# Kernel optimization log

Hardware: AMD Instinct MI355X
Metric: run time of the kernel (lower is better)

## Reference

```python
import jax, jax.numpy as jnp
import numpy as np


def setup_inputs() -> dict:
    key = jax.random.key(0)
    ks = jax.random.split(key, 13)
    B, T, D, H = 64, 2048, 64, 128
    s_in = 1.0 / np.sqrt(H)  # torch RNN/Linear init scale (uniform bound); use scaled normal
    return {
        "x": jax.random.normal(ks[0], (B, T, D), dtype=jnp.float32),
        "W_ih_f": jax.random.normal(ks[1], (H, D), dtype=jnp.float32) * s_in,
        "W_hh_f": jax.random.normal(ks[2], (H, H), dtype=jnp.float32) * s_in,
        "b_ih_f": jax.random.normal(ks[3], (H,), dtype=jnp.float32) * s_in,
        "b_hh_f": jax.random.normal(ks[4], (H,), dtype=jnp.float32) * s_in,
        "W_ih_b": jax.random.normal(ks[5], (H, D), dtype=jnp.float32) * s_in,
        "W_hh_b": jax.random.normal(ks[6], (H, H), dtype=jnp.float32) * s_in,
        "b_ih_b": jax.random.normal(ks[7], (H,), dtype=jnp.float32) * s_in,
        "b_hh_b": jax.random.normal(ks[8], (H,), dtype=jnp.float32) * s_in,
        "fc1_W": jax.random.normal(ks[9], (H, 2 * H), dtype=jnp.float32) * s_in,
        "fc1_b": jax.random.normal(ks[10], (H,), dtype=jnp.float32) * s_in,
        "fc2_W": jax.random.normal(ks[11], (1, H), dtype=jnp.float32) * s_in,
        "fc2_b": jax.random.normal(ks[12], (1,), dtype=jnp.float32) * s_in,
    }


def _rnn_dir(x_proj, W_hh):
    # x_proj: [T, B, H] = x @ W_ih^T + b_ih + b_hh, precomputed (vectorized part)
    # recurrence: h_t = relu(x_proj_t + h_{t-1} @ W_hh^T)
    T, B, H = x_proj.shape
    h0 = jnp.zeros((B, H), dtype=x_proj.dtype)

    def step(h, xp_t):
        h_new = jax.nn.relu(xp_t + h @ W_hh.T)
        return h_new, h_new

    _, hs = jax.lax.scan(step, h0, x_proj)
    return hs  # [T, B, H]


def reference(x, W_ih_f, W_hh_f, b_ih_f, b_hh_f,
              W_ih_b, W_hh_b, b_ih_b, b_hh_b,
              fc1_W, fc1_b, fc2_W, fc2_b):
    # x: [B, T, D]
    xt = jnp.swapaxes(x, 0, 1)  # [T, B, D]
    # forward direction
    xp_f = jnp.einsum('tbd,hd->tbh', xt, W_ih_f) + b_ih_f + b_hh_f
    hs_f = _rnn_dir(xp_f, W_hh_f)  # [T, B, H]
    # backward direction: run over time-reversed input, then reverse outputs
    xp_b = jnp.einsum('tbd,hd->tbh', xt[::-1], W_ih_b) + b_ih_b + b_hh_b
    hs_b = _rnn_dir(xp_b, W_hh_b)[::-1]  # [T, B, H]
    h = jnp.concatenate([hs_f, hs_b], axis=-1)  # [T, B, 2H]
    h = jnp.swapaxes(h, 0, 1)  # [B, T, 2H]
    h = jnp.einsum('bti,oi->bto', h, fc1_W) + fc1_b  # [B, T, H]
    h = jnp.einsum('bti,oi->bto', h, fc2_W) + fc2_b  # [B, T, 1]
    logits = h[..., 0]  # [B, T]
    return jax.nn.log_softmax(logits, axis=1)
```

## Files before the change

kernel.cpp:

```cpp
#include <hip/hip_runtime.h>
#include <hip/hip_bf16.h>

#define T_LEN 2048
#define B_SZ  64
#define D_IN  64
#define H_SZ  128

__global__ __launch_bounds__(256)
void prep_kernel(const float* __restrict__ fc1_W, const float* __restrict__ fc1_b,
                 const float* __restrict__ fc2_W, const float* __restrict__ fc2_b,
                 float* __restrict__ ws)
{
    const int i = threadIdx.x;
    float s = 0.0f;
    #pragma unroll 4
    for (int o = 0; o < 128; ++o) s = fmaf(fc2_W[o], fc1_W[o * 256 + i], s);
    ws[i] = s;

    __shared__ float red[128];
    if (i < 128) red[i] = fc2_W[i] * fc1_b[i];
    __syncthreads();
    if (i == 0) {
        float b = fc2_b[0];
        for (int o = 0; o < 128; ++o) b += red[o];
        ws[256] = b;
    }
}

#define DPP_ADD_F32(v, ctrl)                                                   \
    v += __int_as_float(__builtin_amdgcn_update_dpp(                           \
            0, __float_as_int(v), (ctrl), 0xf, 0xf, true))

__device__ __forceinline__ void chain_barrier() {
    asm volatile("s_waitcnt lgkmcnt(0)" ::: "memory");
    __builtin_amdgcn_s_barrier();
    __builtin_amdgcn_sched_barrier(0);
}


__global__ __launch_bounds__(256, 1)
void brnn_recur(const float* __restrict__ x,
                const float* __restrict__ Wih_f, const float* __restrict__ Whh_f,
                const float* __restrict__ bih_f, const float* __restrict__ bhh_f,
                const float* __restrict__ Wih_b, const float* __restrict__ Whh_b,
                const float* __restrict__ bih_b, const float* __restrict__ bhh_b,
                const float* __restrict__ weff,  float* __restrict__ partbuf)
{
    const int blk  = blockIdx.x;
    const int dir  = blk >> 6;
    const int b    = blk & 63;
    const int tid  = threadIdx.x;
    const int w    = tid >> 6;
    const int l    = tid & 63;
    const int g    = l & 7;
    const int m    = l >> 3;
    const int j0   = w * 32 + m * 4;
    const bool wr  = (g == 7);

    const float* Wih = dir ? Wih_b : Wih_f;
    const float* Whh = dir ? Whh_b : Whh_f;
    const float* bih = dir ? bih_b : bih_f;
    const float* bhh = dir ? bhh_b : bhh_f;

    float whh[64];
    #pragma unroll
    for (int jj = 0; jj < 4; ++jj)
        #pragma unroll
        for (int i = 0; i < 4; ++i)
            ((float4*)whh)[jj * 4 + i] =
                *(const float4*)(Whh + (j0 + jj) * 128 + g * 16 + i * 4);
    float wih[32];
    #pragma unroll
    for (int jj = 0; jj < 4; ++jj)
        #pragma unroll
        for (int i = 0; i < 2; ++i)
            ((float4*)wih)[jj * 2 + i] =
                *(const float4*)(Wih + (j0 + jj) * 64 + g * 8 + i * 4);

    float4 b4 = make_float4(0.f, 0.f, 0.f, 0.f);
    if (g == 0) {
        float4 bi = *(const float4*)(bih + j0);
        float4 bh = *(const float4*)(bhh + j0);
        b4 = make_float4(bi.x + bh.x, bi.y + bh.y, bi.z + bh.z, bi.w + bh.w);
    }
    const float4 w4 = *(const float4*)(weff + dir * 128 + j0);

    __shared__ __align__(16) float hbuf[2][160];
    if (tid < 160) hbuf[0][tid] = 0.0f;
    __syncthreads();

    const float* xbase = x + (size_t)b * T_LEN * D_IN + g * 8;
    float* pout = partbuf + ((size_t)blk * 4 + w) * T_LEN;

    float xq0[8], xq1[8], xq2[8], xq3[8];
    {
        const float4* xp0 = (const float4*)(xbase + (size_t)(dir ? (T_LEN - 1) : 0) * D_IN);
        ((float4*)xq0)[0] = xp0[0];
        ((float4*)xq0)[1] = xp0[1];
        const float4* xp1 = (const float4*)(xbase + (size_t)(dir ? (T_LEN - 2) : 1) * D_IN);
        ((float4*)xq1)[0] = xp1[0];
        ((float4*)xq1)[1] = xp1[1];
    }

    float p_carry = 0.0f;
    int   t_prev  = 0;

    const int hwidx = 40 * w + 4 * m + 4 * (m >> 2);

#define STEP(S, RD, XCUR, XPRE) do {                                           \
        const int s_  = (S);                                                   \
           \
           \
        if (s_ > 0) {                                                          \
            float pr_ = p_carry;                                               \
            DPP_ADD_F32(pr_, 0x111); DPP_ADD_F32(pr_, 0x112);                  \
            DPP_ADD_F32(pr_, 0x114); DPP_ADD_F32(pr_, 0x118);                  \
            DPP_ADD_F32(pr_, 0x142); DPP_ADD_F32(pr_, 0x143);                  \
            if (l == 63) pout[t_prev] = pr_;                                   \
        }                                                                      \
            \
        {                                                                      \
            const int sp_ = (s_ + 2 < T_LEN) ? (s_ + 2) : (T_LEN - 1);         \
            const int tp_ = dir ? (T_LEN - 1 - sp_) : sp_;                     \
            const float4* xp_ = (const float4*)(xbase + (size_t)tp_ * D_IN);   \
            ((float4*)XPRE)[0] = xp_[0];                                       \
            ((float4*)XPRE)[1] = xp_[1];                                       \
        }                                                                      \
            \
        const float4* hp_ = (const float4*)&hbuf[RD][20 * g];                  \
        float4 hv_[4];                                                         \
        _Pragma("unroll") for (int i = 0; i < 4; ++i) hv_[i] = hp_[i];         \
        float a0 = b4.x, a1 = b4.y, a2 = b4.z, a3 = b4.w;                      \
        _Pragma("unroll") for (int i = 0; i < 8; ++i) {                        \
            a0 = fmaf(wih[0 * 8 + i], XCUR[i], a0);                            \
            a1 = fmaf(wih[1 * 8 + i], XCUR[i], a1);                            \
            a2 = fmaf(wih[2 * 8 + i], XCUR[i], a2);                            \
            a3 = fmaf(wih[3 * 8 + i], XCUR[i], a3);                            \
        }                                                                      \
        _Pragma("unroll") for (int i = 0; i < 4; ++i) {                        \
            const float* hq_ = (const float*)&hv_[i];                          \
            _Pragma("unroll") for (int c = 0; c < 4; ++c) {                    \
                a0 = fmaf(whh[0 * 16 + i * 4 + c], hq_[c], a0);                \
                a1 = fmaf(whh[1 * 16 + i * 4 + c], hq_[c], a1);                \
                a2 = fmaf(whh[2 * 16 + i * 4 + c], hq_[c], a2);                \
                a3 = fmaf(whh[3 * 16 + i * 4 + c], hq_[c], a3);                \
            }                                                                  \
        }                                                                      \
             \
        DPP_ADD_F32(a0, 0x111); DPP_ADD_F32(a1, 0x111);                        \
        DPP_ADD_F32(a2, 0x111); DPP_ADD_F32(a3, 0x111);                        \
        DPP_ADD_F32(a0, 0x112); DPP_ADD_F32(a1, 0x112);                        \
        DPP_ADD_F32(a2, 0x112); DPP_ADD_F32(a3, 0x112);                        \
        DPP_ADD_F32(a0, 0x114); DPP_ADD_F32(a1, 0x114);                        \
        DPP_ADD_F32(a2, 0x114); DPP_ADD_F32(a3, 0x114);                        \
        float4 h4_;                                                            \
        h4_.x = fmaxf(a0, 0.0f); h4_.y = fmaxf(a1, 0.0f);                      \
        h4_.z = fmaxf(a2, 0.0f); h4_.w = fmaxf(a3, 0.0f);                      \
        p_carry = 0.0f;                                                        \
        if (wr) {                                                              \
            *(float4*)&hbuf[(RD) ^ 1][hwidx] = h4_;                            \
            p_carry = w4.x * h4_.x + w4.y * h4_.y                              \
                    + w4.z * h4_.z + w4.w * h4_.w;                             \
        }                                                                      \
        t_prev = dir ? (T_LEN - 1 - s_) : s_;                                  \
        chain_barrier();                                                       \
    } while (0)

    #pragma unroll 1
    for (int s = 0; s < T_LEN; s += 4) {
        STEP(s,     0, xq0, xq2);
        STEP(s + 1, 1, xq1, xq3);
        STEP(s + 2, 0, xq2, xq0);
        STEP(s + 3, 1, xq3, xq1);
    }
#undef STEP

    {
        float pr = p_carry;
        DPP_ADD_F32(pr, 0x111); DPP_ADD_F32(pr, 0x112);
        DPP_ADD_F32(pr, 0x114); DPP_ADD_F32(pr, 0x118);
        DPP_ADD_F32(pr, 0x142); DPP_ADD_F32(pr, 0x143);
        if (l == 63) pout[t_prev] = pr;
    }
}

__global__ __launch_bounds__(256)
void brnn_lsm(const float* __restrict__ partbuf, const float* __restrict__ ws,
              float* __restrict__ out)
{
    const int b   = blockIdx.x;
    const int tid = threadIdx.x;
    __shared__ float lg[T_LEN];
    __shared__ float red[8];

    const float beff = ws[256];

    float lmax = -3.0e38f;
    for (int t = tid; t < T_LEN; t += 256) {
        float s = beff;
        #pragma unroll
        for (int dw = 0; dw < 8; ++dw) {
            const int dir = dw >> 2, wv = dw & 3;
            s += partbuf[(((size_t)(dir * 64 + b)) * 4 + wv) * T_LEN + t];
        }
        lg[t] = s;
        lmax = fmaxf(lmax, s);
    }
    #pragma unroll
    for (int mm = 1; mm <= 32; mm <<= 1) lmax = fmaxf(lmax, __shfl_xor(lmax, mm));
    if ((tid & 63) == 0) red[tid >> 6] = lmax;
    __syncthreads();
    const float bmax = fmaxf(fmaxf(red[0], red[1]), fmaxf(red[2], red[3]));

    float lsum = 0.0f;
    for (int t = tid; t < T_LEN; t += 256) lsum += expf(lg[t] - bmax);
    #pragma unroll
    for (int mm = 1; mm <= 32; mm <<= 1) lsum += __shfl_xor(lsum, mm);
    if ((tid & 63) == 0) red[4 + (tid >> 6)] = lsum;
    __syncthreads();
    const float lse = bmax + logf(red[4] + red[5] + red[6] + red[7]);

    for (int t = tid; t < T_LEN; t += 256)
        out[(size_t)b * T_LEN + t] = lg[t] - lse;
}

extern "C" void kernel_launch(void* const* d_in, const int* in_sizes, int n_in,
                              void* d_out, int out_size, void* d_ws, size_t ws_size,
                              hipStream_t stream)
{
    const float* x     = (const float*)d_in[0];
    const float* Wih_f = (const float*)d_in[1];
    const float* Whh_f = (const float*)d_in[2];
    const float* bih_f = (const float*)d_in[3];
    const float* bhh_f = (const float*)d_in[4];
    const float* Wih_b = (const float*)d_in[5];
    const float* Whh_b = (const float*)d_in[6];
    const float* bih_b = (const float*)d_in[7];
    const float* bhh_b = (const float*)d_in[8];
    const float* fc1_W = (const float*)d_in[9];
    const float* fc1_b = (const float*)d_in[10];
    const float* fc2_W = (const float*)d_in[11];
    const float* fc2_b = (const float*)d_in[12];
    float* out = (float*)d_out;

    float* wsf  = (float*)d_ws;
    float* part = wsf + 512;

    hipLaunchKernelGGL(prep_kernel, dim3(1), dim3(256), 0, stream,
                       fc1_W, fc1_b, fc2_W, fc2_b, wsf);
    hipLaunchKernelGGL(brnn_recur, dim3(128), dim3(256), 0, stream,
                       x, Wih_f, Whh_f, bih_f, bhh_f,
                       Wih_b, Whh_b, bih_b, bhh_b, wsf, part);
    hipLaunchKernelGGL(brnn_lsm, dim3(64), dim3(256), 0, stream,
                       part, wsf, out);
}
```

Before: 800.6 us.

## Precompute input projection in a separate GEMM kernel before the recurrence

Adds an xp_gemm kernel that computes x·W_ih^T + biases for both directions into a large workspace buffer. The recurrent kernel then loads one float4 of precomputed projection per step instead of doing 32 FMAs against x. The aim is to shorten the per-step serial chain. It also trims the p_carry DPP reduction from six to three steps, because only g==7 lanes hold nonzero values. The cost is an extra kernel that writes and later reads about 128 MB of workspace. A fallback to the old fused path runs when the workspace is too small.

```diff
diff --git a/kernel.cpp b/kernel.cpp
--- a/kernel.cpp
+++ b/kernel.cpp
@@ -27,6 +27,56 @@
     }
 }
 
+__global__ __launch_bounds__(128)
+void xp_gemm(const float* __restrict__ x,
+             const float* __restrict__ Wih_f, const float* __restrict__ bih_f,
+             const float* __restrict__ bhh_f,
+             const float* __restrict__ Wih_b, const float* __restrict__ bih_b,
+             const float* __restrict__ bhh_b,
+             float* __restrict__ xp)
+{
+    const int blk = blockIdx.x;
+    const int dir = blk >> 10;
+    const int b   = (blk >> 4) & 63;
+    const int c   = blk & 15;
+    const int j   = threadIdx.x;
+
+    const float* Wih = dir ? Wih_b : Wih_f;
+    const float* bih = dir ? bih_b : bih_f;
+    const float* bhh = dir ? bhh_b : bhh_f;
+
+    __shared__ __align__(16) float xs[128][64];
+    const float4* xsrc = (const float4*)(x + ((size_t)b * T_LEN + c * 128) * D_IN);
+    float4* xdst = (float4*)&xs[0][0];
+    #pragma unroll
+    for (int i = 0; i < 16; ++i) xdst[threadIdx.x + i * 128] = xsrc[threadIdx.x + i * 128];
+
+    float wr[64];
+    #pragma unroll
+    for (int i = 0; i < 16; ++i) ((float4*)wr)[i] = ((const float4*)(Wih + j * 64))[i];
+    const float bj = bih[j] + bhh[j];
+    __syncthreads();
+
+    float* xpo = xp + (((size_t)(dir * 64 + b)) * T_LEN + c * 128) * H_SZ + j;
+    for (int tt = 0; tt < 128; ++tt) {
+        const float4* xr = (const float4*)&xs[tt][0];
+        float a0 = bj, a1 = 0.f, a2 = 0.f, a3 = 0.f;
+        #pragma unroll
+        for (int i = 0; i < 16; i += 4) {
+            float4 v0 = xr[i], v1 = xr[i + 1], v2 = xr[i + 2], v3 = xr[i + 3];
+            a0 = fmaf(wr[4*i+ 0], v0.x, a0); a0 = fmaf(wr[4*i+ 1], v0.y, a0);
+            a0 = fmaf(wr[4*i+ 2], v0.z, a0); a0 = fmaf(wr[4*i+ 3], v0.w, a0);
+            a1 = fmaf(wr[4*i+ 4], v1.x, a1); a1 = fmaf(wr[4*i+ 5], v1.y, a1);
+            a1 = fmaf(wr[4*i+ 6], v1.z, a1); a1 = fmaf(wr[4*i+ 7], v1.w, a1);
+            a2 = fmaf(wr[4*i+ 8], v2.x, a2); a2 = fmaf(wr[4*i+ 9], v2.y, a2);
+            a2 = fmaf(wr[4*i+10], v2.z, a2); a2 = fmaf(wr[4*i+11], v2.w, a2);
+            a3 = fmaf(wr[4*i+12], v3.x, a3); a3 = fmaf(wr[4*i+13], v3.y, a3);
+            a3 = fmaf(wr[4*i+14], v3.z, a3); a3 = fmaf(wr[4*i+15], v3.w, a3);
+        }
+        xpo[(size_t)tt * H_SZ] = (a0 + a1) + (a2 + a3);
+    }
+}
+
 #define DPP_ADD_F32(v, ctrl)                                                   \
     v += __int_as_float(__builtin_amdgcn_update_dpp(                           \
             0, __float_as_int(v), (ctrl), 0xf, 0xf, true))
@@ -39,12 +89,9 @@
 
 
 __global__ __launch_bounds__(256, 1)
-void brnn_recur(const float* __restrict__ x,
-                const float* __restrict__ Wih_f, const float* __restrict__ Whh_f,
-                const float* __restrict__ bih_f, const float* __restrict__ bhh_f,
-                const float* __restrict__ Wih_b, const float* __restrict__ Whh_b,
-                const float* __restrict__ bih_b, const float* __restrict__ bhh_b,
-                const float* __restrict__ weff,  float* __restrict__ partbuf)
+void brnn_recur_xp(const float* __restrict__ xp,
+                   const float* __restrict__ Whh_f, const float* __restrict__ Whh_b,
+                   const float* __restrict__ weff,  float* __restrict__ partbuf)
 {
     const int blk  = blockIdx.x;
     const int dir  = blk >> 6;
@@ -57,10 +104,7 @@
     const int j0   = w * 32 + m * 4;
     const bool wr  = (g == 7);
 
-    const float* Wih = dir ? Wih_b : Wih_f;
     const float* Whh = dir ? Whh_b : Whh_f;
-    const float* bih = dir ? bih_b : bih_f;
-    const float* bhh = dir ? bhh_b : bhh_f;
 
     float whh[64];
     #pragma unroll
@@ -69,74 +113,49 @@
         for (int i = 0; i < 4; ++i)
             ((float4*)whh)[jj * 4 + i] =
                 *(const float4*)(Whh + (j0 + jj) * 128 + g * 16 + i * 4);
-    float wih[32];
-    #pragma unroll
-    for (int jj = 0; jj < 4; ++jj)
-        #pragma unroll
-        for (int i = 0; i < 2; ++i)
-            ((float4*)wih)[jj * 2 + i] =
-                *(const float4*)(Wih + (j0 + jj) * 64 + g * 8 + i * 4);
-
-    float4 b4 = make_float4(0.f, 0.f, 0.f, 0.f);
-    if (g == 0) {
-        float4 bi = *(const float4*)(bih + j0);
-        float4 bh = *(const float4*)(bhh + j0);
-        b4 = make_float4(bi.x + bh.x, bi.y + bh.y, bi.z + bh.z, bi.w + bh.w);
-    }
+
     const float4 w4 = *(const float4*)(weff + dir * 128 + j0);
 
     __shared__ __align__(16) float hbuf[2][160];
     if (tid < 160) hbuf[0][tid] = 0.0f;
     __syncthreads();
 
-    const float* xbase = x + (size_t)b * T_LEN * D_IN + g * 8;
+    const float* xpbase = xp + ((size_t)(dir * 64 + b)) * T_LEN * H_SZ + j0;
     float* pout = partbuf + ((size_t)blk * 4 + w) * T_LEN;
 
-    float xq0[8], xq1[8], xq2[8], xq3[8];
-    {
-        const float4* xp0 = (const float4*)(xbase + (size_t)(dir ? (T_LEN - 1) : 0) * D_IN);
-        ((float4*)xq0)[0] = xp0[0];
-        ((float4*)xq0)[1] = xp0[1];
-        const float4* xp1 = (const float4*)(xbase + (size_t)(dir ? (T_LEN - 2) : 1) * D_IN);
-        ((float4*)xq1)[0] = xp1[0];
-        ((float4*)xq1)[1] = xp1[1];
-    }
+    float4 xq0, xq1, xq2, xq3;
+    xq0 = *(const float4*)(xpbase + (size_t)(dir ? (T_LEN - 1) : 0) * H_SZ);
+    xq1 = *(const float4*)(xpbase + (size_t)(dir ? (T_LEN - 2) : 1) * H_SZ);
 
     float p_carry = 0.0f;
     int   t_prev  = 0;
 
     const int hwidx = 40 * w + 4 * m + 4 * (m >> 2);
 
-#define STEP(S, RD, XCUR, XPRE) do {                                           \
+#define STEP(S, RD, XPC, XPN) do {                                             \
         const int s_  = (S);                                                   \
-           \
-           \
+                 \
         if (s_ > 0) {                                                          \
             float pr_ = p_carry;                                               \
-            DPP_ADD_F32(pr_, 0x111); DPP_ADD_F32(pr_, 0x112);                  \
-            DPP_ADD_F32(pr_, 0x114); DPP_ADD_F32(pr_, 0x118);                  \
-            DPP_ADD_F32(pr_, 0x142); DPP_ADD_F32(pr_, 0x143);                  \
+            DPP_ADD_F32(pr_, 0x118);     \
+            DPP_ADD_F32(pr_, 0x142);         \
+            DPP_ADD_F32(pr_, 0x143);             \
             if (l == 63) pout[t_prev] = pr_;                                   \
         }                                                                      \
-            \
+                                                 \
         {                                                                      \
             const int sp_ = (s_ + 2 < T_LEN) ? (s_ + 2) : (T_LEN - 1);         \
             const int tp_ = dir ? (T_LEN - 1 - sp_) : sp_;                     \
-            const float4* xp_ = (const float4*)(xbase + (size_t)tp_ * D_IN);   \
-            ((float4*)XPRE)[0] = xp_[0];                                       \
-            ((float4*)XPRE)[1] = xp_[1];                                       \
-        }                                                                      \
-            \
+            XPN = *(const float4*)(xpbase + (size_t)tp_ * H_SZ);               \
+        }                                                                      \
+                                        \
         const float4* hp_ = (const float4*)&hbuf[RD][20 * g];                  \
         float4 hv_[4];                                                         \
         _Pragma("unroll") for (int i = 0; i < 4; ++i) hv_[i] = hp_[i];         \
-        float a0 = b4.x, a1 = b4.y, a2 = b4.z, a3 = b4.w;                      \
-        _Pragma("unroll") for (int i = 0; i < 8; ++i) {                        \
-            a0 = fmaf(wih[0 * 8 + i], XCUR[i], a0);                            \
-            a1 = fmaf(wih[1 * 8 + i], XCUR[i], a1);                            \
-            a2 = fmaf(wih[2 * 8 + i], XCUR[i], a2);                            \
-            a3 = fmaf(wih[3 * 8 + i], XCUR[i], a3);                            \
-        }                                                                      \
+        float a0 = (g == 0) ? XPC.x : 0.0f;                                    \
+        float a1 = (g == 0) ? XPC.y : 0.0f;                                    \
+        float a2 = (g == 0) ? XPC.z : 0.0f;                                    \
+        float a3 = (g == 0) ? XPC.w : 0.0f;                                    \
         _Pragma("unroll") for (int i = 0; i < 4; ++i) {                        \
             const float* hq_ = (const float*)&hv_[i];                          \
             _Pragma("unroll") for (int c = 0; c < 4; ++c) {                    \
@@ -177,9 +196,146 @@
 
     {
         float pr = p_carry;
-        DPP_ADD_F32(pr, 0x111); DPP_ADD_F32(pr, 0x112);
-        DPP_ADD_F32(pr, 0x114); DPP_ADD_F32(pr, 0x118);
-        DPP_ADD_F32(pr, 0x142); DPP_ADD_F32(pr, 0x143);
+        DPP_ADD_F32(pr, 0x118);
+        DPP_ADD_F32(pr, 0x142);
+        DPP_ADD_F32(pr, 0x143);
+        if (l == 63) pout[t_prev] = pr;
+    }
+}
+
+__global__ __launch_bounds__(256, 1)
+void brnn_recur_fb(const float* __restrict__ x,
+                   const float* __restrict__ Wih_f, const float* __restrict__ Whh_f,
+                   const float* __restrict__ bih_f, const float* __restrict__ bhh_f,
+                   const float* __restrict__ Wih_b, const float* __restrict__ Whh_b,
+                   const float* __restrict__ bih_b, const float* __restrict__ bhh_b,
+                   const float* __restrict__ weff,  float* __restrict__ partbuf)
+{
+    const int blk  = blockIdx.x;
+    const int dir  = blk >> 6;
+    const int b    = blk & 63;
+    const int tid  = threadIdx.x;
+    const int w    = tid >> 6;
+    const int l    = tid & 63;
+    const int g    = l & 7;
+    const int m    = l >> 3;
+    const int j0   = w * 32 + m * 4;
+    const bool wr  = (g == 7);
+
+    const float* Wih = dir ? Wih_b : Wih_f;
+    const float* Whh = dir ? Whh_b : Whh_f;
+    const float* bih = dir ? bih_b : bih_f;
+    const float* bhh = dir ? bhh_b : bhh_f;
+
+    float whh[64];
+    #pragma unroll
+    for (int jj = 0; jj < 4; ++jj)
+        #pragma unroll
+        for (int i = 0; i < 4; ++i)
+            ((float4*)whh)[jj * 4 + i] =
+                *(const float4*)(Whh + (j0 + jj) * 128 + g * 16 + i * 4);
+    float wih[32];
+    #pragma unroll
+    for (int jj = 0; jj < 4; ++jj)
+        #pragma unroll
+        for (int i = 0; i < 2; ++i)
+            ((float4*)wih)[jj * 2 + i] =
+                *(const float4*)(Wih + (j0 + jj) * 64 + g * 8 + i * 4);
+
+    float4 b4 = make_float4(0.f, 0.f, 0.f, 0.f);
+    if (g == 0) {
+        float4 bi = *(const float4*)(bih + j0);
+        float4 bh = *(const float4*)(bhh + j0);
+        b4 = make_float4(bi.x + bh.x, bi.y + bh.y, bi.z + bh.z, bi.w + bh.w);
+    }
+    const float4 w4 = *(const float4*)(weff + dir * 128 + j0);
+
+    __shared__ __align__(16) float hbuf[2][160];
+    if (tid < 160) hbuf[0][tid] = 0.0f;
+    __syncthreads();
+
+    const float* xbase = x + (size_t)b * T_LEN * D_IN + g * 8;
+    float* pout = partbuf + ((size_t)blk * 4 + w) * T_LEN;
+
+    float xq0[8], xq1[8], xq2[8], xq3[8];
+    {
+        const float4* xp0 = (const float4*)(xbase + (size_t)(dir ? (T_LEN - 1) : 0) * D_IN);
+        ((float4*)xq0)[0] = xp0[0];
+        ((float4*)xq0)[1] = xp0[1];
+        const float4* xp1 = (const float4*)(xbase + (size_t)(dir ? (T_LEN - 2) : 1) * D_IN);
+        ((float4*)xq1)[0] = xp1[0];
+        ((float4*)xq1)[1] = xp1[1];
+    }
+
+    float p_carry = 0.0f;
+    int   t_prev  = 0;
+    const int hwidx = 40 * w + 4 * m + 4 * (m >> 2);
+
+#define STEP(S, RD, XCUR, XPRE) do {                                           \
+        const int s_  = (S);                                                   \
+        if (s_ > 0) {                                                          \
+            float pr_ = p_carry;                                               \
+            DPP_ADD_F32(pr_, 0x118); DPP_ADD_F32(pr_, 0x142);                  \
+            DPP_ADD_F32(pr_, 0x143);                                           \
+            if (l == 63) pout[t_prev] = pr_;                                   \
+        }                                                                      \
+        {                                                                      \
+            const int sp_ = (s_ + 2 < T_LEN) ? (s_ + 2) : (T_LEN - 1);         \
+            const int tp_ = dir ? (T_LEN - 1 - sp_) : sp_;                     \
+            const float4* xp_ = (const float4*)(xbase + (size_t)tp_ * D_IN);   \
+            ((float4*)XPRE)[0] = xp_[0];                                       \
+            ((float4*)XPRE)[1] = xp_[1];                                       \
+        }                                                                      \
+        const float4* hp_ = (const float4*)&hbuf[RD][20 * g];                  \
+        float4 hv_[4];                                                         \
+        _Pragma("unroll") for (int i = 0; i < 4; ++i) hv_[i] = hp_[i];         \
+        float a0 = b4.x, a1 = b4.y, a2 = b4.z, a3 = b4.w;                      \
+        _Pragma("unroll") for (int i = 0; i < 8; ++i) {                        \
+            a0 = fmaf(wih[0 * 8 + i], XCUR[i], a0);                            \
+            a1 = fmaf(wih[1 * 8 + i], XCUR[i], a1);                            \
+            a2 = fmaf(wih[2 * 8 + i], XCUR[i], a2);                            \
+            a3 = fmaf(wih[3 * 8 + i], XCUR[i], a3);                            \
+        }                                                                      \
+        _Pragma("unroll") for (int i = 0; i < 4; ++i) {                        \
+            const float* hq_ = (const float*)&hv_[i];                          \
+            _Pragma("unroll") for (int c = 0; c < 4; ++c) {                    \
+                a0 = fmaf(whh[0 * 16 + i * 4 + c], hq_[c], a0);                \
+                a1 = fmaf(whh[1 * 16 + i * 4 + c], hq_[c], a1);                \
+                a2 = fmaf(whh[2 * 16 + i * 4 + c], hq_[c], a2);                \
+                a3 = fmaf(whh[3 * 16 + i * 4 + c], hq_[c], a3);                \
+            }                                                                  \
+        }                                                                      \
+        DPP_ADD_F32(a0, 0x111); DPP_ADD_F32(a1, 0x111);                        \
+        DPP_ADD_F32(a2, 0x111); DPP_ADD_F32(a3, 0x111);                        \
+        DPP_ADD_F32(a0, 0x112); DPP_ADD_F32(a1, 0x112);                        \
+        DPP_ADD_F32(a2, 0x112); DPP_ADD_F32(a3, 0x112);                        \
+        DPP_ADD_F32(a0, 0x114); DPP_ADD_F32(a1, 0x114);                        \
+        DPP_ADD_F32(a2, 0x114); DPP_ADD_F32(a3, 0x114);                        \
+        float4 h4_;                                                            \
+        h4_.x = fmaxf(a0, 0.0f); h4_.y = fmaxf(a1, 0.0f);                      \
+        h4_.z = fmaxf(a2, 0.0f); h4_.w = fmaxf(a3, 0.0f);                      \
+        p_carry = 0.0f;                                                        \
+        if (wr) {                                                              \
+            *(float4*)&hbuf[(RD) ^ 1][hwidx] = h4_;                            \
+            p_carry = w4.x * h4_.x + w4.y * h4_.y                              \
+                    + w4.z * h4_.z + w4.w * h4_.w;                             \
+        }                                                                      \
+        t_prev = dir ? (T_LEN - 1 - s_) : s_;                                  \
+        chain_barrier();                                                       \
+    } while (0)
+
+    #pragma unroll 1
+    for (int s = 0; s < T_LEN; s += 4) {
+        STEP(s,     0, xq0, xq2);
+        STEP(s + 1, 1, xq1, xq3);
+        STEP(s + 2, 0, xq2, xq0);
+        STEP(s + 3, 1, xq3, xq1);
+    }
+#undef STEP
+
+    {
+        float pr = p_carry;
+        DPP_ADD_F32(pr, 0x118); DPP_ADD_F32(pr, 0x142); DPP_ADD_F32(pr, 0x143);
         if (l == 63) pout[t_prev] = pr;
     }
 }
@@ -243,14 +399,27 @@
     const float* fc2_b = (const float*)d_in[12];
     float* out = (float*)d_out;
 
-    float* wsf  = (float*)d_ws;
-    float* part = wsf + 512;
+    float* wsf = (float*)d_ws;
+    const size_t part_off   = 512;
+    const size_t part_elems = (size_t)2 * 64 * 4 * T_LEN;
+    const size_t xp_off     = part_off + part_elems;
+    const size_t xp_elems   = (size_t)2 * 64 * T_LEN * H_SZ;
+    float* part = wsf + part_off;
+    float* xpbf = wsf + xp_off;
+    const bool big_ws = ws_size >= (xp_off + xp_elems) * sizeof(float);
 
     hipLaunchKernelGGL(prep_kernel, dim3(1), dim3(256), 0, stream,
                        fc1_W, fc1_b, fc2_W, fc2_b, wsf);
-    hipLaunchKernelGGL(brnn_recur, dim3(128), dim3(256), 0, stream,
-                       x, Wih_f, Whh_f, bih_f, bhh_f,
-                       Wih_b, Whh_b, bih_b, bhh_b, wsf, part);
+    if (big_ws) {
+        hipLaunchKernelGGL(xp_gemm, dim3(2048), dim3(128), 0, stream,
+                           x, Wih_f, bih_f, bhh_f, Wih_b, bih_b, bhh_b, xpbf);
+        hipLaunchKernelGGL(brnn_recur_xp, dim3(128), dim3(256), 0, stream,
+                           xpbf, Whh_f, Whh_b, wsf, part);
+    } else {
+        hipLaunchKernelGGL(brnn_recur_fb, dim3(128), dim3(256), 0, stream,
+                           x, Wih_f, Whh_f, bih_f, bhh_f,
+                           Wih_b, Whh_b, bih_b, bhh_b, wsf, part);
+    }
     hipLaunchKernelGGL(brnn_lsm, dim3(64), dim3(256), 0, stream,
                        part, wsf, out);
 }
```

New measurement: 800.5 us. About the same (-0.0%).

## Precompute input projection in a separate GEMM kernel and slim the recurrence loop

Applied to the files above, without the earlier changes.

Adds an xp_gemm kernel that computes x@W_ih^T plus both biases for all timesteps and both directions into workspace. The recurrence kernel then only loads the precomputed projections, packed as 8-step float4 batches per row. This takes the input-projection FMAs off the serial critical path. It also relaxes the per-step barrier so the compiler can schedule across it, shortens the partial-sum DPP reduction, and batches the partial-sum stores. In exchange it needs a large workspace (about 128 MB) and an extra pass through memory, and falls back to the old kernel when the workspace is too small.

```diff
diff --git a/kernel.cpp b/kernel.cpp
--- a/kernel.cpp
+++ b/kernel.cpp
@@ -27,6 +27,44 @@
     }
 }
 
+__global__ __launch_bounds__(256)
+void xp_gemm(const float* __restrict__ x,
+             const float* __restrict__ Wih_f, const float* __restrict__ bih_f,
+             const float* __restrict__ bhh_f,
+             const float* __restrict__ Wih_b, const float* __restrict__ bih_b,
+             const float* __restrict__ bhh_b,
+             float* __restrict__ xp)
+{
+    const int blk = blockIdx.x;
+    const int dir = blk >> 9;
+    const int b   = (blk >> 3) & 63;
+    const int c   = blk & 7;
+    const int t   = c * 256 + threadIdx.x;
+
+    const float* __restrict__ Wih = dir ? Wih_b : Wih_f;
+    const float* __restrict__ bih = dir ? bih_b : bih_f;
+    const float* __restrict__ bhh = dir ? bhh_b : bhh_f;
+
+    float xr[64];
+    const float4* xsrc = (const float4*)(x + ((size_t)b * T_LEN + t) * D_IN);
+    #pragma unroll
+    for (int i = 0; i < 16; ++i) ((float4*)xr)[i] = xsrc[i];
+
+    float* xpo = xp + ((size_t)(dir * 64 + b) * H_SZ) * T_LEN + t;
+    #pragma unroll 2
+    for (int j = 0; j < 128; j += 2) {
+        float a0 = bih[j] + bhh[j];
+        float a1 = bih[j + 1] + bhh[j + 1];
+        #pragma unroll
+        for (int d = 0; d < 64; ++d) {
+            a0 = fmaf(Wih[j * 64 + d],       xr[d], a0);
+            a1 = fmaf(Wih[(j + 1) * 64 + d], xr[d], a1);
+        }
+        xpo[(size_t)j * T_LEN]       = a0;
+        xpo[(size_t)(j + 1) * T_LEN] = a1;
+    }
+}
+
 #define DPP_ADD_F32(v, ctrl)                                                   \
     v += __int_as_float(__builtin_amdgcn_update_dpp(                           \
             0, __float_as_int(v), (ctrl), 0xf, 0xf, true))
@@ -34,17 +72,163 @@
 __device__ __forceinline__ void chain_barrier() {
     asm volatile("s_waitcnt lgkmcnt(0)" ::: "memory");
     __builtin_amdgcn_s_barrier();
+    asm volatile("" ::: "memory");
+}
+__device__ __forceinline__ void chain_barrier_strict() {
+    asm volatile("s_waitcnt lgkmcnt(0)" ::: "memory");
+    __builtin_amdgcn_s_barrier();
     __builtin_amdgcn_sched_barrier(0);
 }
 
 
+template<int DIR>
+__device__ __forceinline__
+void recur_chain(const float* __restrict__ xp, const float* __restrict__ Whh,
+                 const float* __restrict__ weff, float* __restrict__ partbuf,
+                 int b, int blk, float (*hbuf)[160])
+{
+    const int tid = threadIdx.x;
+    const int w   = tid >> 6;
+    const int l   = tid & 63;
+    const int g   = l & 7;
+    const int m   = l >> 3;
+    const int j0  = w * 32 + m * 4;
+    const bool wr = (g == 7);
+
+    float whh[64];
+    #pragma unroll
+    for (int jj = 0; jj < 4; ++jj)
+        #pragma unroll
+        for (int i = 0; i < 4; ++i)
+            ((float4*)whh)[jj * 4 + i] =
+                *(const float4*)(Whh + (j0 + jj) * H_SZ + g * 16 + i * 4);
+
+    const float4 w4 = *(const float4*)(weff + DIR * H_SZ + j0);
+
+    const float4* rd0 = (const float4*)&hbuf[0][20 * g];
+    const float4* rd1 = (const float4*)&hbuf[1][20 * g];
+    const int hwidx = 40 * w + 4 * m + 4 * (m >> 2);
+    float* wp1 = &hbuf[1][hwidx];
+    float* wp0 = &hbuf[0][hwidx];
+
+    const size_t rowbase = ((size_t)(DIR * 64 + b) * H_SZ + j0) * (size_t)T_LEN;
+    const int t0 = DIR ? (T_LEN - 1) : 0;
+    const float* xs0 = xp + rowbase + (size_t)0 * T_LEN + t0;
+    const float* xs1 = xp + rowbase + (size_t)1 * T_LEN + t0;
+    const float* xs2 = xp + rowbase + (size_t)2 * T_LEN + t0;
+    const float* xs3 = xp + rowbase + (size_t)3 * T_LEN + t0;
+
+    float* pst = partbuf + ((size_t)blk * 4 + w) * T_LEN + (DIR ? (T_LEN - 8) : 0);
+
+    float4 XA[8], XB[8];
+    #pragma unroll
+    for (int k = 0; k < 8; ++k) {
+        const int o = DIR ? -k : k;
+        XA[k].x = xs0[o]; XA[k].y = xs1[o]; XA[k].z = xs2[o]; XA[k].w = xs3[o];
+    }
+    const ptrdiff_t adv = DIR ? -8 : 8;
+    xs0 += adv; xs1 += adv; xs2 += adv; xs3 += adv;
+
+    float ps[8];
+
+#define KSTEP(K, XCUR, XNXT) do {                                              \
+        float4 hv0, hv1, hv2, hv3;                                             \
+        if ((K) & 1) { hv0 = rd1[0]; hv1 = rd1[1]; hv2 = rd1[2]; hv3 = rd1[3]; } \
+        else         { hv0 = rd0[0]; hv1 = rd0[1]; hv2 = rd0[2]; hv3 = rd0[3]; } \
+        {       \
+            const int o_ = DIR ? -(K) : (K);                                   \
+            XNXT[K].x = xs0[o_]; XNXT[K].y = xs1[o_];                          \
+            XNXT[K].z = xs2[o_]; XNXT[K].w = xs3[o_];                          \
+        }                                                                      \
+        float a0 = (g == 0) ? XCUR[K].x : 0.0f;                                \
+        float a1 = (g == 0) ? XCUR[K].y : 0.0f;                                \
+        float a2 = (g == 0) ? XCUR[K].z : 0.0f;                                \
+        float a3 = (g == 0) ? XCUR[K].w : 0.0f;                                \
+        _Pragma("unroll") for (int c = 0; c < 4; ++c) {                        \
+            const float h_ = ((const float*)&hv0)[c];                          \
+            a0 = fmaf(whh[ 0 + c], h_, a0); a1 = fmaf(whh[16 + c], h_, a1);    \
+            a2 = fmaf(whh[32 + c], h_, a2); a3 = fmaf(whh[48 + c], h_, a3);    \
+        }                                                                      \
+        _Pragma("unroll") for (int c = 0; c < 4; ++c) {                        \
+            const float h_ = ((const float*)&hv1)[c];                          \
+            a0 = fmaf(whh[ 4 + c], h_, a0); a1 = fmaf(whh[20 + c], h_, a1);    \
+            a2 = fmaf(whh[36 + c], h_, a2); a3 = fmaf(whh[52 + c], h_, a3);    \
+        }                                                                      \
+        _Pragma("unroll") for (int c = 0; c < 4; ++c) {                        \
+            const float h_ = ((const float*)&hv2)[c];                          \
+            a0 = fmaf(whh[ 8 + c], h_, a0); a1 = fmaf(whh[24 + c], h_, a1);    \
+            a2 = fmaf(whh[40 + c], h_, a2); a3 = fmaf(whh[56 + c], h_, a3);    \
+        }                                                                      \
+        _Pragma("unroll") for (int c = 0; c < 4; ++c) {                        \
+            const float h_ = ((const float*)&hv3)[c];                          \
+            a0 = fmaf(whh[12 + c], h_, a0); a1 = fmaf(whh[28 + c], h_, a1);    \
+            a2 = fmaf(whh[44 + c], h_, a2); a3 = fmaf(whh[60 + c], h_, a3);    \
+        }                                                                      \
+        DPP_ADD_F32(a0, 0x111); DPP_ADD_F32(a1, 0x111);                        \
+        DPP_ADD_F32(a2, 0x111); DPP_ADD_F32(a3, 0x111);                        \
+        DPP_ADD_F32(a0, 0x112); DPP_ADD_F32(a1, 0x112);                        \
+        DPP_ADD_F32(a2, 0x112); DPP_ADD_F32(a3, 0x112);                        \
+        DPP_ADD_F32(a0, 0x114); DPP_ADD_F32(a1, 0x114);                        \
+        DPP_ADD_F32(a2, 0x114); DPP_ADD_F32(a3, 0x114);                        \
+        float4 h4;                                                             \
+        h4.x = fmaxf(a0, 0.0f); h4.y = fmaxf(a1, 0.0f);                        \
+        h4.z = fmaxf(a2, 0.0f); h4.w = fmaxf(a3, 0.0f);                        \
+        if (wr) *(float4*)(((K) & 1) ? wp0 : wp1) = h4;                        \
+        float pv = wr ? (w4.x * h4.x + w4.y * h4.y                             \
+                       + w4.z * h4.z + w4.w * h4.w) : 0.0f;                    \
+        DPP_ADD_F32(pv, 0x118); DPP_ADD_F32(pv, 0x142); DPP_ADD_F32(pv, 0x143);\
+        ps[K] = pv;                                                            \
+        chain_barrier();                                                       \
+    } while (0)
+
+#define ITER8(XCUR, XNXT) do {                                                 \
+        KSTEP(0, XCUR, XNXT); KSTEP(1, XCUR, XNXT);                            \
+        KSTEP(2, XCUR, XNXT); KSTEP(3, XCUR, XNXT);                            \
+        KSTEP(4, XCUR, XNXT); KSTEP(5, XCUR, XNXT);                            \
+        KSTEP(6, XCUR, XNXT); KSTEP(7, XCUR, XNXT);                            \
+        if (l == 63) {                                                         \
+            float4 v0, v1;                                                     \
+            if (DIR) { v0 = make_float4(ps[7], ps[6], ps[5], ps[4]);           \
+                       v1 = make_float4(ps[3], ps[2], ps[1], ps[0]); }         \
+            else     { v0 = make_float4(ps[0], ps[1], ps[2], ps[3]);           \
+                       v1 = make_float4(ps[4], ps[5], ps[6], ps[7]); }         \
+            *(float4*)pst = v0; *(float4*)(pst + 4) = v1;                      \
+        }                                                                      \
+        xs0 += adv; xs1 += adv; xs2 += adv; xs3 += adv;                        \
+        pst += DIR ? -8 : 8;                                                   \
+    } while (0)
+
+    #pragma unroll 1
+    for (int it = 0; it < T_LEN / 16; ++it) {
+        ITER8(XA, XB);
+        ITER8(XB, XA);
+    }
+#undef ITER8
+#undef KSTEP
+}
+
 __global__ __launch_bounds__(256, 1)
-void brnn_recur(const float* __restrict__ x,
-                const float* __restrict__ Wih_f, const float* __restrict__ Whh_f,
-                const float* __restrict__ bih_f, const float* __restrict__ bhh_f,
-                const float* __restrict__ Wih_b, const float* __restrict__ Whh_b,
-                const float* __restrict__ bih_b, const float* __restrict__ bhh_b,
-                const float* __restrict__ weff,  float* __restrict__ partbuf)
+void brnn_recur_xp(const float* __restrict__ xp,
+                   const float* __restrict__ Whh_f, const float* __restrict__ Whh_b,
+                   const float* __restrict__ weff,  float* __restrict__ partbuf)
+{
+    __shared__ __align__(16) float hbuf[2][160];
+    const int blk = blockIdx.x;
+    const int dir = blk >> 6;
+    const int b   = blk & 63;
+    if (threadIdx.x < 160) hbuf[0][threadIdx.x] = 0.0f;
+    __syncthreads();
+    if (dir == 0) recur_chain<0>(xp, Whh_f, weff, partbuf, b, blk, hbuf);
+    else          recur_chain<1>(xp, Whh_b, weff, partbuf, b, blk, hbuf);
+}
+
+__global__ __launch_bounds__(256, 1)
+void brnn_recur_fb(const float* __restrict__ x,
+                   const float* __restrict__ Wih_f, const float* __restrict__ Whh_f,
+                   const float* __restrict__ bih_f, const float* __restrict__ bhh_f,
+                   const float* __restrict__ Wih_b, const float* __restrict__ Whh_b,
+                   const float* __restrict__ bih_b, const float* __restrict__ bhh_b,
+                   const float* __restrict__ weff,  float* __restrict__ partbuf)
 {
     const int blk  = blockIdx.x;
     const int dir  = blk >> 6;
@@ -104,21 +288,16 @@
 
     float p_carry = 0.0f;
     int   t_prev  = 0;
-
     const int hwidx = 40 * w + 4 * m + 4 * (m >> 2);
 
 #define STEP(S, RD, XCUR, XPRE) do {                                           \
         const int s_  = (S);                                                   \
-           \
-           \
         if (s_ > 0) {                                                          \
             float pr_ = p_carry;                                               \
-            DPP_ADD_F32(pr_, 0x111); DPP_ADD_F32(pr_, 0x112);                  \
-            DPP_ADD_F32(pr_, 0x114); DPP_ADD_F32(pr_, 0x118);                  \
-            DPP_ADD_F32(pr_, 0x142); DPP_ADD_F32(pr_, 0x143);                  \
+            DPP_ADD_F32(pr_, 0x118); DPP_ADD_F32(pr_, 0x142);                  \
+            DPP_ADD_F32(pr_, 0x143);                                           \
             if (l == 63) pout[t_prev] = pr_;                                   \
         }                                                                      \
-            \
         {                                                                      \
             const int sp_ = (s_ + 2 < T_LEN) ? (s_ + 2) : (T_LEN - 1);         \
             const int tp_ = dir ? (T_LEN - 1 - sp_) : sp_;                     \
@@ -126,7 +305,6 @@
             ((float4*)XPRE)[0] = xp_[0];                                       \
             ((float4*)XPRE)[1] = xp_[1];                                       \
         }                                                                      \
-            \
         const float4* hp_ = (const float4*)&hbuf[RD][20 * g];                  \
         float4 hv_[4];                                                         \
         _Pragma("unroll") for (int i = 0; i < 4; ++i) hv_[i] = hp_[i];         \
@@ -146,7 +324,6 @@
                 a3 = fmaf(whh[3 * 16 + i * 4 + c], hq_[c], a3);                \
             }                                                                  \
         }                                                                      \
-             \
         DPP_ADD_F32(a0, 0x111); DPP_ADD_F32(a1, 0x111);                        \
         DPP_ADD_F32(a2, 0x111); DPP_ADD_F32(a3, 0x111);                        \
         DPP_ADD_F32(a0, 0x112); DPP_ADD_F32(a1, 0x112);                        \
@@ -163,7 +340,7 @@
                     + w4.z * h4_.z + w4.w * h4_.w;                             \
         }                                                                      \
         t_prev = dir ? (T_LEN - 1 - s_) : s_;                                  \
-        chain_barrier();                                                       \
+        chain_barrier_strict();                                                \
     } while (0)
 
     #pragma unroll 1
@@ -177,9 +354,7 @@
 
     {
         float pr = p_carry;
-        DPP_ADD_F32(pr, 0x111); DPP_ADD_F32(pr, 0x112);
-        DPP_ADD_F32(pr, 0x114); DPP_ADD_F32(pr, 0x118);
-        DPP_ADD_F32(pr, 0x142); DPP_ADD_F32(pr, 0x143);
+        DPP_ADD_F32(pr, 0x118); DPP_ADD_F32(pr, 0x142); DPP_ADD_F32(pr, 0x143);
         if (l == 63) pout[t_prev] = pr;
     }
 }
@@ -243,14 +418,27 @@
     const float* fc2_b = (const float*)d_in[12];
     float* out = (float*)d_out;
 
-    float* wsf  = (float*)d_ws;
-    float* part = wsf + 512;
+    float* wsf = (float*)d_ws;
+    const size_t part_off   = 512;
+    const size_t part_elems = (size_t)2 * 64 * 4 * T_LEN;
+    const size_t xp_off     = part_off + part_elems;
+    const size_t xp_elems   = (size_t)2 * 64 * T_LEN * H_SZ;
+    float* part = wsf + part_off;
+    float* xpbf = wsf + xp_off;
+    const bool big_ws = ws_size >= (xp_off + xp_elems) * sizeof(float);
 
     hipLaunchKernelGGL(prep_kernel, dim3(1), dim3(256), 0, stream,
                        fc1_W, fc1_b, fc2_W, fc2_b, wsf);
-    hipLaunchKernelGGL(brnn_recur, dim3(128), dim3(256), 0, stream,
-                       x, Wih_f, Whh_f, bih_f, bhh_f,
-                       Wih_b, Whh_b, bih_b, bhh_b, wsf, part);
+    if (big_ws) {
+        hipLaunchKernelGGL(xp_gemm, dim3(1024), dim3(256), 0, stream,
+                           x, Wih_f, bih_f, bhh_f, Wih_b, bih_b, bhh_b, xpbf);
+        hipLaunchKernelGGL(brnn_recur_xp, dim3(128), dim3(256), 0, stream,
+                           xpbf, Whh_f, Whh_b, wsf, part);
+    } else {
+        hipLaunchKernelGGL(brnn_recur_fb, dim3(128), dim3(256), 0, stream,
+                           x, Wih_f, Whh_f, bih_f, bhh_f,
+                           Wih_b, Whh_b, bih_b, bhh_b, wsf, part);
+    }
     hipLaunchKernelGGL(brnn_lsm, dim3(64), dim3(256), 0, stream,
                        part, wsf, out);
 }
```

New measurement: 937.7 us. 1.17x slower.

## Precompute input projection with a GEMM and interleave both directions per block

Applied to the files above, without the earlier changes.

Adds a separate tiled GEMM kernel that computes x@W_ih^T plus the biases for both directions into a large workspace buffer. The recurrence kernel then runs the forward and backward chains together in one block, interleaving two independent dependency chains so each can hide the other's latency, and it shares one barrier per step. This uses 64 blocks instead of 128 and adds about 128MB of extra global traffic. The partial-sum DPP reduction is also shortened, and the original path is kept as a fallback when the workspace is too small.

```diff
diff --git a/kernel.cpp b/kernel.cpp
--- a/kernel.cpp
+++ b/kernel.cpp
@@ -27,6 +27,85 @@
     }
 }
 
+__global__ __launch_bounds__(256, 2)
+void xp_gemm(const float* __restrict__ x,
+             const float* __restrict__ Wih_f, const float* __restrict__ bih_f,
+             const float* __restrict__ bhh_f,
+             const float* __restrict__ Wih_b, const float* __restrict__ bih_b,
+             const float* __restrict__ bhh_b,
+             float* __restrict__ xp)
+{
+    const int blk = blockIdx.x;
+    const int dir = blk >> 11;
+    const int b   = (blk >> 5) & 63;
+    const int tc  = blk & 31;
+    const int tid = threadIdx.x;
+
+    const float* __restrict__ Wih = dir ? Wih_b : Wih_f;
+    const float* __restrict__ bih = dir ? bih_b : bih_f;
+    const float* __restrict__ bhh = dir ? bhh_b : bhh_f;
+
+    __shared__ __align__(16) float xs[64][68];
+    __shared__ __align__(16) float wsd[128][68];
+    __shared__ float bs[128];
+
+    {
+        const float4* src = (const float4*)(x + ((size_t)b * T_LEN + tc * 64) * D_IN);
+        #pragma unroll
+        for (int r = 0; r < 4; ++r) {
+            int q = tid + 256 * r;
+            float4 v = src[q];
+            *(float4*)&xs[q >> 4][(q & 15) * 4] = v;
+        }
+        const float4* wsrc = (const float4*)Wih;
+        #pragma unroll
+        for (int r = 0; r < 8; ++r) {
+            int q = tid + 256 * r;
+            float4 v = wsrc[q];
+            *(float4*)&wsd[q >> 4][(q & 15) * 4] = v;
+        }
+        if (tid < 128) bs[tid] = bih[tid] + bhh[tid];
+    }
+    __syncthreads();
+
+    const int jg = tid & 15;
+    const int tg = tid >> 4;
+
+    float acc[8][4];
+    #pragma unroll
+    for (int jj = 0; jj < 8; ++jj)
+        #pragma unroll
+        for (int tt = 0; tt < 4; ++tt) acc[jj][tt] = 0.0f;
+
+    #pragma unroll 2
+    for (int kc = 0; kc < 16; ++kc) {
+        float4 xv[4];
+        #pragma unroll
+        for (int tt = 0; tt < 4; ++tt)
+            xv[tt] = *(const float4*)&xs[tg + 16 * tt][kc * 4];
+        #pragma unroll
+        for (int jj = 0; jj < 8; ++jj) {
+            float4 wv = *(const float4*)&wsd[jg + 16 * jj][kc * 4];
+            #pragma unroll
+            for (int tt = 0; tt < 4; ++tt) {
+                acc[jj][tt] = fmaf(wv.x, xv[tt].x, acc[jj][tt]);
+                acc[jj][tt] = fmaf(wv.y, xv[tt].y, acc[jj][tt]);
+                acc[jj][tt] = fmaf(wv.z, xv[tt].z, acc[jj][tt]);
+                acc[jj][tt] = fmaf(wv.w, xv[tt].w, acc[jj][tt]);
+            }
+        }
+    }
+
+    float* xpo = xp + ((size_t)(dir * 64 + b) * T_LEN + tc * 64) * H_SZ;
+    #pragma unroll
+    for (int jj = 0; jj < 8; ++jj) {
+        const float bj = bs[jg + 16 * jj];
+        #pragma unroll
+        for (int tt = 0; tt < 4; ++tt)
+            xpo[(size_t)(tg + 16 * tt) * H_SZ + jg + 16 * jj] = acc[jj][tt] + bj;
+    }
+}
+
 #define DPP_ADD_F32(v, ctrl)                                                   \
     v += __int_as_float(__builtin_amdgcn_update_dpp(                           \
             0, __float_as_int(v), (ctrl), 0xf, 0xf, true))
@@ -34,17 +113,147 @@
 __device__ __forceinline__ void chain_barrier() {
     asm volatile("s_waitcnt lgkmcnt(0)" ::: "memory");
     __builtin_amdgcn_s_barrier();
+    asm volatile("" ::: "memory");
+}
+__device__ __forceinline__ void chain_barrier_strict() {
+    asm volatile("s_waitcnt lgkmcnt(0)" ::: "memory");
+    __builtin_amdgcn_s_barrier();
     __builtin_amdgcn_sched_barrier(0);
 }
 
 
+__device__ __forceinline__
+void chain_step(const float* __restrict__ wh, float4& XC,
+                const float4* __restrict__ rdp, float* __restrict__ wrp,
+                const float4 w4, float* __restrict__ po, int tt,
+                const float* __restrict__ pref, int g, bool wr, int l)
+{
+    float4 hv[4];
+    #pragma unroll
+    for (int i = 0; i < 4; ++i) hv[i] = rdp[i];
+
+    float a0 = (g == 0) ? XC.x : 0.0f;
+    float a1 = (g == 0) ? XC.y : 0.0f;
+    float a2 = (g == 0) ? XC.z : 0.0f;
+    float a3 = (g == 0) ? XC.w : 0.0f;
+    XC = *(const float4*)pref;
+
+    #pragma unroll
+    for (int i = 0; i < 4; ++i) {
+        #pragma unroll
+        for (int c = 0; c < 4; ++c) {
+            const float h_ = ((const float*)&hv[i])[c];
+            a0 = fmaf(wh[ 0 + i * 4 + c], h_, a0);
+            a1 = fmaf(wh[16 + i * 4 + c], h_, a1);
+            a2 = fmaf(wh[32 + i * 4 + c], h_, a2);
+            a3 = fmaf(wh[48 + i * 4 + c], h_, a3);
+        }
+    }
+    DPP_ADD_F32(a0, 0x111); DPP_ADD_F32(a1, 0x111);
+    DPP_ADD_F32(a2, 0x111); DPP_ADD_F32(a3, 0x111);
+    DPP_ADD_F32(a0, 0x112); DPP_ADD_F32(a1, 0x112);
+    DPP_ADD_F32(a2, 0x112); DPP_ADD_F32(a3, 0x112);
+    DPP_ADD_F32(a0, 0x114); DPP_ADD_F32(a1, 0x114);
+    DPP_ADD_F32(a2, 0x114); DPP_ADD_F32(a3, 0x114);
+
+    float4 h4;
+    h4.x = fmaxf(a0, 0.0f); h4.y = fmaxf(a1, 0.0f);
+    h4.z = fmaxf(a2, 0.0f); h4.w = fmaxf(a3, 0.0f);
+
+    float pv = 0.0f;
+    if (wr) {
+        *(float4*)wrp = h4;
+        pv = fmaf(w4.x, h4.x, fmaf(w4.y, h4.y, fmaf(w4.z, h4.z, w4.w * h4.w)));
+    }
+    DPP_ADD_F32(pv, 0x118);
+    DPP_ADD_F32(pv, 0x142);
+    DPP_ADD_F32(pv, 0x143);
+    if (l == 63) po[tt] = pv;
+}
+
 __global__ __launch_bounds__(256, 1)
-void brnn_recur(const float* __restrict__ x,
-                const float* __restrict__ Wih_f, const float* __restrict__ Whh_f,
-                const float* __restrict__ bih_f, const float* __restrict__ bhh_f,
-                const float* __restrict__ Wih_b, const float* __restrict__ Whh_b,
-                const float* __restrict__ bih_b, const float* __restrict__ bhh_b,
-                const float* __restrict__ weff,  float* __restrict__ partbuf)
+void brnn_recur_dual(const float* __restrict__ xp,
+                     const float* __restrict__ Whh_f, const float* __restrict__ Whh_b,
+                     const float* __restrict__ weff,  float* __restrict__ partbuf)
+{
+    const int b   = blockIdx.x;
+    const int tid = threadIdx.x;
+    const int w   = tid >> 6;
+    const int l   = tid & 63;
+    const int g   = l & 7;
+    const int m   = l >> 3;
+    const int j0  = w * 32 + m * 4;
+    const bool wr = (g == 7);
+
+    float whF[64], whB[64];
+    #pragma unroll
+    for (int jj = 0; jj < 4; ++jj)
+        #pragma unroll
+        for (int i = 0; i < 4; ++i) {
+            ((float4*)whF)[jj * 4 + i] =
+                *(const float4*)(Whh_f + (j0 + jj) * H_SZ + g * 16 + i * 4);
+            ((float4*)whB)[jj * 4 + i] =
+                *(const float4*)(Whh_b + (j0 + jj) * H_SZ + g * 16 + i * 4);
+        }
+
+    const float4 w4F = *(const float4*)(weff + j0);
+    const float4 w4B = *(const float4*)(weff + H_SZ + j0);
+
+    __shared__ __align__(16) float hF[2][160], hB[2][160];
+    if (tid < 160) { hF[0][tid] = 0.0f; hB[0][tid] = 0.0f; }
+    __syncthreads();
+
+    const float* xpF = xp + (size_t)b * T_LEN * H_SZ + j0;
+    const float* xpB = xp + (size_t)(64 + b) * T_LEN * H_SZ + j0;
+    float* poF = partbuf + ((size_t)b * 4 + w) * T_LEN;
+    float* poB = partbuf + ((size_t)(64 + b) * 4 + w) * T_LEN;
+
+    const float4* rF0 = (const float4*)&hF[0][20 * g];
+    const float4* rF1 = (const float4*)&hF[1][20 * g];
+    const float4* rB0 = (const float4*)&hB[0][20 * g];
+    const float4* rB1 = (const float4*)&hB[1][20 * g];
+    const int hwidx = 40 * w + 4 * m + 4 * (m >> 2);
+    float* wF0 = &hF[0][hwidx];
+    float* wF1 = &hF[1][hwidx];
+    float* wB0 = &hB[0][hwidx];
+    float* wB1 = &hB[1][hwidx];
+
+    float4 xF0 = *(const float4*)(xpF);
+    float4 xF1 = *(const float4*)(xpF + (size_t)1 * H_SZ);
+    float4 xB0 = *(const float4*)(xpB + (size_t)(T_LEN - 1) * H_SZ);
+    float4 xB1 = *(const float4*)(xpB + (size_t)(T_LEN - 2) * H_SZ);
+
+    #pragma unroll 1
+    for (int s = 0; s < T_LEN; s += 2) {
+        {
+            const int spF = (s + 2 < T_LEN) ? s + 2 : T_LEN - 1;
+            const int spB = (s + 2 < T_LEN) ? (T_LEN - 3 - s) : 0;
+            chain_step(whF, xF0, rF0, wF1, w4F, poF, s,
+                       xpF + (size_t)spF * H_SZ, g, wr, l);
+            chain_step(whB, xB0, rB0, wB1, w4B, poB, T_LEN - 1 - s,
+                       xpB + (size_t)spB * H_SZ, g, wr, l);
+            chain_barrier();
+        }
+        {
+            const int sq  = s + 1;
+            const int sqF = (sq + 2 < T_LEN) ? sq + 2 : T_LEN - 1;
+            const int sqB = (sq + 2 < T_LEN) ? (T_LEN - 3 - sq) : 0;
+            chain_step(whF, xF1, rF1, wF0, w4F, poF, sq,
+                       xpF + (size_t)sqF * H_SZ, g, wr, l);
+            chain_step(whB, xB1, rB1, wB0, w4B, poB, T_LEN - 1 - sq,
+                       xpB + (size_t)sqB * H_SZ, g, wr, l);
+            chain_barrier();
+        }
+    }
+}
+
+__global__ __launch_bounds__(256, 1)
+void brnn_recur_fb(const float* __restrict__ x,
+                   const float* __restrict__ Wih_f, const float* __restrict__ Whh_f,
+                   const float* __restrict__ bih_f, const float* __restrict__ bhh_f,
+                   const float* __restrict__ Wih_b, const float* __restrict__ Whh_b,
+                   const float* __restrict__ bih_b, const float* __restrict__ bhh_b,
+                   const float* __restrict__ weff,  float* __restrict__ partbuf)
 {
     const int blk  = blockIdx.x;
     const int dir  = blk >> 6;
@@ -104,21 +313,16 @@
 
     float p_carry = 0.0f;
     int   t_prev  = 0;
-
     const int hwidx = 40 * w + 4 * m + 4 * (m >> 2);
 
 #define STEP(S, RD, XCUR, XPRE) do {                                           \
         const int s_  = (S);                                                   \
-           \
-           \
         if (s_ > 0) {                                                          \
             float pr_ = p_carry;                                               \
-            DPP_ADD_F32(pr_, 0x111); DPP_ADD_F32(pr_, 0x112);                  \
-            DPP_ADD_F32(pr_, 0x114); DPP_ADD_F32(pr_, 0x118);                  \
-            DPP_ADD_F32(pr_, 0x142); DPP_ADD_F32(pr_, 0x143);                  \
+            DPP_ADD_F32(pr_, 0x118); DPP_ADD_F32(pr_, 0x142);                  \
+            DPP_ADD_F32(pr_, 0x143);                                           \
             if (l == 63) pout[t_prev] = pr_;                                   \
         }                                                                      \
-            \
         {                                                                      \
             const int sp_ = (s_ + 2 < T_LEN) ? (s_ + 2) : (T_LEN - 1);         \
             const int tp_ = dir ? (T_LEN - 1 - sp_) : sp_;                     \
@@ -126,7 +330,6 @@
             ((float4*)XPRE)[0] = xp_[0];                                       \
             ((float4*)XPRE)[1] = xp_[1];                                       \
         }                                                                      \
-            \
         const float4* hp_ = (const float4*)&hbuf[RD][20 * g];                  \
         float4 hv_[4];                                                         \
         _Pragma("unroll") for (int i = 0; i < 4; ++i) hv_[i] = hp_[i];         \
@@ -146,7 +349,6 @@
                 a3 = fmaf(whh[3 * 16 + i * 4 + c], hq_[c], a3);                \
             }                                                                  \
         }                                                                      \
-             \
         DPP_ADD_F32(a0, 0x111); DPP_ADD_F32(a1, 0x111);                        \
         DPP_ADD_F32(a2, 0x111); DPP_ADD_F32(a3, 0x111);                        \
         DPP_ADD_F32(a0, 0x112); DPP_ADD_F32(a1, 0x112);                        \
@@ -163,7 +365,7 @@
                     + w4.z * h4_.z + w4.w * h4_.w;                             \
         }                                                                      \
         t_prev = dir ? (T_LEN - 1 - s_) : s_;                                  \
-        chain_barrier();                                                       \
+        chain_barrier_strict();                                                \
     } while (0)
 
     #pragma unroll 1
@@ -177,9 +379,7 @@
 
     {
         float pr = p_carry;
-        DPP_ADD_F32(pr, 0x111); DPP_ADD_F32(pr, 0x112);
-        DPP_ADD_F32(pr, 0x114); DPP_ADD_F32(pr, 0x118);
-        DPP_ADD_F32(pr, 0x142); DPP_ADD_F32(pr, 0x143);
+        DPP_ADD_F32(pr, 0x118); DPP_ADD_F32(pr, 0x142); DPP_ADD_F32(pr, 0x143);
         if (l == 63) pout[t_prev] = pr;
     }
 }
@@ -243,14 +443,27 @@
     const float* fc2_b = (const float*)d_in[12];
     float* out = (float*)d_out;
 
-    float* wsf  = (float*)d_ws;
-    float* part = wsf + 512;
+    float* wsf = (float*)d_ws;
+    const size_t part_off   = 512;
+    const size_t part_elems = (size_t)2 * 64 * 4 * T_LEN;
+    const size_t xp_off     = part_off + part_elems;
+    const size_t xp_elems   = (size_t)2 * 64 * T_LEN * H_SZ;
+    float* part = wsf + part_off;
+    float* xpbf = wsf + xp_off;
+    const bool big_ws = ws_size >= (xp_off + xp_elems) * sizeof(float);
 
     hipLaunchKernelGGL(prep_kernel, dim3(1), dim3(256), 0, stream,
                        fc1_W, fc1_b, fc2_W, fc2_b, wsf);
-    hipLaunchKernelGGL(brnn_recur, dim3(128), dim3(256), 0, stream,
-                       x, Wih_f, Whh_f, bih_f, bhh_f,
-                       Wih_b, Whh_b, bih_b, bhh_b, wsf, part);
+    if (big_ws) {
+        hipLaunchKernelGGL(xp_gemm, dim3(4096), dim3(256), 0, stream,
+                           x, Wih_f, bih_f, bhh_f, Wih_b, bih_b, bhh_b, xpbf);
+        hipLaunchKernelGGL(brnn_recur_dual, dim3(64), dim3(256), 0, stream,
+                           xpbf, Whh_f, Whh_b, wsf, part);
+    } else {
+        hipLaunchKernelGGL(brnn_recur_fb, dim3(128), dim3(256), 0, stream,
+                           x, Wih_f, Whh_f, bih_f, bhh_f,
+                           Wih_b, Whh_b, bih_b, bhh_b, wsf, part);
+    }
     hipLaunchKernelGGL(brnn_lsm, dim3(64), dim3(256), 0, stream,
                        part, wsf, out);
 }
```

After: 1.181 ms. 1.48x slower.
